# Performance work log

Hardware: AMD Instinct MI355X
Metric: run time of the kernel (lower is better)

## Reference

```python
import jax, jax.numpy as jnp
import numpy as np

N_HEAD = 12
N_EMBD = 768


def setup_inputs() -> dict:
    key = jax.random.key(0)
    k1, k2, k3, k4, k5 = jax.random.split(key, 5)
    B, T, C = 4, 2048, N_EMBD
    s = 0.02
    x = jax.random.normal(k1, (B, T, C), dtype=jnp.float32)
    w_attn = jax.random.normal(k2, (C, 3 * C), dtype=jnp.float32) * s
    b_attn = jnp.zeros((3 * C,), dtype=jnp.float32)
    w_proj = jax.random.normal(k3, (C, C), dtype=jnp.float32) * s
    b_proj = jnp.zeros((C,), dtype=jnp.float32)
    return {"x": x, "w_attn": w_attn, "b_attn": b_attn, "w_proj": w_proj, "b_proj": b_proj}


def reference(x, w_attn, b_attn, w_proj, b_proj):
    # dropout omitted (eval mode / dropout=0.0)
    B, T, C = x.shape
    H = N_HEAD
    D = C // H  # head dim
    qkv = x @ w_attn + b_attn                      # [B,T,3C]
    q, k, v = jnp.split(qkv, 3, axis=-1)
    q = q.reshape(B, T, H, D).transpose(0, 2, 1, 3)  # [B,H,T,D]
    k = k.reshape(B, T, H, D).transpose(0, 2, 1, 3)
    v = v.reshape(B, T, H, D).transpose(0, 2, 1, 3)
    att = jnp.einsum('bhqd,bhkd->bhqk', q, k) * (1.0 / np.sqrt(D))  # [B,H,T,T]
    causal = jnp.tril(jnp.ones((T, T), dtype=bool))
    att = jnp.where(causal[None, None], att, -jnp.inf)
    att = jax.nn.softmax(att, axis=-1)
    y = jnp.einsum('bhqk,bhkd->bhqd', att, v)      # [B,H,T,D]
    y = y.transpose(0, 2, 1, 3).reshape(B, T, C)
    return y @ w_proj + b_proj
```

## Files before the change

### kernel.cpp

```cpp
#include <hip/hip_runtime.h>
#include <stdint.h>

typedef unsigned short ushort_t;

#define T_SEQ 2048
#define BATCH 4
#define NHEAD 12
#define CEMB 768
#define HDIM 64
#define C3 2304

__device__ __forceinline__ ushort_t f2b_hw(float f) {
  union { __bf16 h; ushort_t u; } p;
  p.h = (__bf16)f;
  return p.u;
}
__device__ __forceinline__ uint32_t pkbf16(float lo, float hi) {
  union { __bf16 h[2]; uint32_t u; } p;
  p.h[0] = (__bf16)lo; p.h[1] = (__bf16)hi;
  return p.u;
}

typedef __attribute__((address_space(3))) unsigned int lds_u32_t;
typedef const __attribute__((address_space(1))) unsigned int glb_u32_t;
__device__ __forceinline__ void async_cp16(const void* g, void* l) {
  __builtin_amdgcn_global_load_lds((glb_u32_t*)g, (lds_u32_t*)l, 16, 0, 0);
}

__global__ __launch_bounds__(256) void prep_k(const float* __restrict__ x, ushort_t* __restrict__ xb,
                                              const float* __restrict__ wa, ushort_t* __restrict__ wT,
                                              const float* __restrict__ wp, ushort_t* __restrict__ wpT) {
  const int blk = blockIdx.x;
  const int tid = threadIdx.x;
  if (blk < 3072) {
    const int i = blk * 256 + tid;
    float4 a = ((const float4*)x)[2 * i];
    float4 b = ((const float4*)x)[2 * i + 1];
    uint4 v;
    v.x = pkbf16(a.x, a.y); v.y = pkbf16(a.z, a.w);
    v.z = pkbf16(b.x, b.y); v.w = pkbf16(b.z, b.w);
    ((uint4*)xb)[i] = v;
    return;
  }
  __shared__ ushort_t tile[32][33];
  const float* in; ushort_t* out; int R, C, bx, by;
  if (blk < 4800) {
    const int t = blk - 3072;
    in = wa; out = wT; R = CEMB; C = C3;
    bx = t % 72; by = t / 72;
  } else {
    const int t = blk - 4800;
    in = wp; out = wpT; R = CEMB; C = CEMB;
    bx = t % 24; by = t / 24;
  }
  const int tx = tid & 31, ty = tid >> 5;
  const int c0 = bx * 32, r0 = by * 32;
  for (int i = ty; i < 32; i += 8)
    tile[i][tx] = f2b_hw(in[(size_t)(r0 + i) * C + c0 + tx]);
  __syncthreads();
  for (int i = ty; i < 32; i += 8)
    out[(size_t)(c0 + i) * R + r0 + tx] = tile[tx][i];
}

typedef __bf16 bf16x8 __attribute__((ext_vector_type(8)));
typedef float f32x4 __attribute__((ext_vector_type(4)));

template <bool OUTF, int BM>
__global__ __launch_bounds__(256) void gemm_bt(const ushort_t* __restrict__ A,
                                               const ushort_t* __restrict__ Bt,
                                               const float* __restrict__ bias,
                                               void* __restrict__ Cv,
                                               int M, int N, int K) {
  constexpr int TM = BM / 32;
  __shared__ ushort_t As[BM * 32];
  __shared__ ushort_t Bs[128 * 32];
  const int tid = threadIdx.x;
  const int m0 = blockIdx.y * BM, n0 = blockIdx.x * 128;
  const int wid = tid >> 6, lane = tid & 63;
  const int quad = lane >> 4, l15 = lane & 15;
  const int wm = (wid >> 1) * (BM / 2), wn = (wid & 1) * 64;
  f32x4 acc[TM][4] = {};

  const int e0 = tid * 8;
  const int r0s = e0 >> 5, c0s = e0 & 31;
  const int e1 = e0 + 2048;
  const int r1s = e1 >> 5, c1s = e1 & 31;

  for (int k0 = 0; k0 < K; k0 += 32) {
    __syncthreads();
    async_cp16(&A[(size_t)(m0 + r0s) * K + k0 + c0s], &As[e0]);
    if constexpr (BM == 128)
      async_cp16(&A[(size_t)(m0 + r1s) * K + k0 + c1s], &As[e1]);
    async_cp16(&Bt[(size_t)(n0 + r0s) * K + k0 + c0s], &Bs[e0]);
    async_cp16(&Bt[(size_t)(n0 + r1s) * K + k0 + c1s], &Bs[e1]);
    __syncthreads();
    bf16x8 af[TM], bfr[4];
#pragma unroll
    for (int t = 0; t < TM; t++)
      af[t] = *(const bf16x8*)&As[(wm + t * 16 + l15) * 32 + quad * 8];
#pragma unroll
    for (int t = 0; t < 4; t++)
      bfr[t] = *(const bf16x8*)&Bs[(wn + t * 16 + l15) * 32 + quad * 8];
#pragma unroll
    for (int tm = 0; tm < TM; tm++)
#pragma unroll
      for (int tn = 0; tn < 4; tn++)
        acc[tm][tn] = __builtin_amdgcn_mfma_f32_16x16x32_bf16(af[tm], bfr[tn], acc[tm][tn], 0, 0, 0);
  }

#pragma unroll
  for (int tm = 0; tm < TM; tm++) {
    const int row = m0 + wm + tm * 16 + quad * 4;
#pragma unroll
    for (int tn = 0; tn < 4; tn++) {
      const int col = n0 + wn + tn * 16 + l15;
      const float bv = bias[col];
#pragma unroll
      for (int rr = 0; rr < 4; rr++) {
        if constexpr (OUTF)
          ((float*)Cv)[(size_t)(row + rr) * N + col] = acc[tm][tn][rr] + bv;
        else
          ((ushort_t*)Cv)[(size_t)(row + rr) * N + col] = f2b_hw(acc[tm][tn][rr] + bv);
      }
    }
  }
}

#define PSTR 72

__device__ __forceinline__ void commit_v(ushort_t* __restrict__ vt, int vd0, int vpair,
                                         uint4 pV0, uint4 pV1) {
  union { uint32_t u[4]; uint4 v; } a, c;
  a.v = pV0; c.v = pV1;
#pragma unroll
  for (int j = 0; j < 8; j++) {
    uint32_t pk = __builtin_amdgcn_perm(c.u[j >> 1], a.u[j >> 1],
                                        (j & 1) ? 0x07060302u : 0x05040100u);
    *(uint32_t*)&vt[(vd0 + j) * PSTR + 2 * vpair] = pk;
  }
}

__global__ __launch_bounds__(256) void attn_mfma_k(const ushort_t* __restrict__ qkv,
                                                   ushort_t* __restrict__ y) {
  __shared__ ushort_t Ksm[2][2][64 * 32];
  __shared__ ushort_t Vt[2][64 * PSTR];
  __shared__ ushort_t Plds[4][32 * PSTR];

  const int jj = blockIdx.x;
  const int h = blockIdx.y, b = blockIdx.z;
  const int tid = threadIdx.x;
  const int w = tid >> 6, lane = tid & 63;
  const int quad = lane >> 4, l15 = lane & 15;

  const int e0 = tid * 8;
  const int k_key = e0 >> 5, k_col = e0 & 31;
  const int vpair = tid & 31, vd0 = (tid >> 5) * 8;
  const ushort_t* kbase = qkv + ((size_t)(b * T_SEQ) + k_key) * C3 + CEMB + h * HDIM + k_col;
  const ushort_t* vbase = qkv + ((size_t)(b * T_SEQ) + 2 * vpair) * C3 + 2 * CEMB + h * HDIM + vd0;
  const size_t step = (size_t)64 * C3;

  int koff[4], voff[4], poffR[2], poffW[2];
#pragma unroll
  for (int m = 0; m < 4; m++) koff[m] = (m * 16 + l15) * 32 + quad * 8;
#pragma unroll
  for (int nd = 0; nd < 4; nd++) voff[nd] = (nd * 16 + l15) * PSTR + quad * 8;
#pragma unroll
  for (int n = 0; n < 2; n++) {
    poffR[n] = (n * 16 + l15) * PSTR + quad * 8;
    poffW[n] = (n * 16 + l15) * PSTR + quad * 4;
  }

  const float C2 = 0.18033688011112042f;

  for (int ph = 0; ph < 2; ++ph) {
    const int qt = ph ? (15 - jj) : jj;
    const int nkt = 2 * qt + 2;
    const int qw = qt * 128 + w * 32;

    bf16x8 qB[2][2];
#pragma unroll
    for (int n = 0; n < 2; n++)
#pragma unroll
      for (int kb = 0; kb < 2; kb++)
        qB[n][kb] = *(const bf16x8*)&qkv[((size_t)(b * T_SEQ + qw + n * 16 + l15)) * C3 +
                                         h * HDIM + kb * 32 + quad * 8];

    f32x4 o2[4][2] = {};
    float m_i[2] = {-3e38f, -3e38f}, l_i[2] = {0.f, 0.f};

    __syncthreads();

    const ushort_t* kp = kbase;
    const ushort_t* vp = vbase;
    uint4 pV0 = *(const uint4*)vp, pV1 = *(const uint4*)(vp + C3);
    async_cp16(kp, &Ksm[0][0][e0]);
    async_cp16(kp + 32, &Ksm[0][1][e0]);
    commit_v(Vt[0], vd0, vpair, pV0, pV1);
    vp += step;
    pV0 = *(const uint4*)vp; pV1 = *(const uint4*)(vp + C3);

    for (int kt = 0; kt < nkt; ++kt) {
      __syncthreads();
      if (kt + 1 < nkt) {
        const int nb = (kt + 1) & 1;
        kp += step;
        async_cp16(kp, &Ksm[nb][0][e0]);
        async_cp16(kp + 32, &Ksm[nb][1][e0]);
        commit_v(Vt[nb], vd0, vpair, pV0, pV1);
        if (kt + 2 < nkt) {
          vp += step;
          pV0 = *(const uint4*)vp; pV1 = *(const uint4*)(vp + C3);
        }
      }
      const int cb = kt & 1;

      if (kt * 64 <= qw + 31) {
        bf16x8 kA[4][2];
#pragma unroll
        for (int m = 0; m < 4; m++) {
          kA[m][0] = *(const bf16x8*)&Ksm[cb][0][koff[m]];
          kA[m][1] = *(const bf16x8*)&Ksm[cb][1][koff[m]];
        }
        f32x4 st[4][2] = {};
#pragma unroll
        for (int m = 0; m < 4; m++)
#pragma unroll
          for (int n = 0; n < 2; n++) {
            st[m][n] = __builtin_amdgcn_mfma_f32_16x16x32_bf16(kA[m][0], qB[n][0], st[m][n], 0, 0, 0);
            st[m][n] = __builtin_amdgcn_mfma_f32_16x16x32_bf16(kA[m][1], qB[n][1], st[m][n], 0, 0, 0);
          }

        if (kt * 64 + 63 > qw) {
#pragma unroll
          for (int m = 0; m < 4; m++)
#pragma unroll
            for (int r = 0; r < 4; r++) {
              const int keyg = kt * 64 + m * 16 + quad * 4 + r;
#pragma unroll
              for (int n = 0; n < 2; n++) {
                const int qg = qw + n * 16 + l15;
                if (keyg > qg) st[m][n][r] = -3e38f;
              }
            }
        }

        float al[2];
#pragma unroll
        for (int n = 0; n < 2; n++) {
          float mx = st[0][n][0];
#pragma unroll
          for (int m = 0; m < 4; m++)
#pragma unroll
            for (int r = 0; r < 4; r++) mx = fmaxf(mx, st[m][n][r]);
          mx = fmaxf(mx, __shfl_xor(mx, 16, 64));
          mx = fmaxf(mx, __shfl_xor(mx, 32, 64));
          const float mn = fmaxf(m_i[n], mx);
          al[n] = exp2f((m_i[n] - mn) * C2);
          m_i[n] = mn;
          const float mnc = mn * C2;
          float ls = 0.f;
#pragma unroll
          for (int m = 0; m < 4; m++)
#pragma unroll
            for (int r = 0; r < 4; r++) {
              float p = exp2f(fmaf(st[m][n][r], C2, -mnc));
              st[m][n][r] = p;
              ls += p;
            }
          ls += __shfl_xor(ls, 16, 64);
          ls += __shfl_xor(ls, 32, 64);
          l_i[n] = l_i[n] * al[n] + ls;
        }

#pragma unroll
        for (int n = 0; n < 2; n++) {
#pragma unroll
          for (int m = 0; m < 4; m++) {
            uint2 pk;
            pk.x = pkbf16(st[m][n][0], st[m][n][1]);
            pk.y = pkbf16(st[m][n][2], st[m][n][3]);
            *(uint2*)&Plds[w][poffW[n] + m * 16] = pk;
          }
#pragma unroll
          for (int nd = 0; nd < 4; nd++)
#pragma unroll
            for (int r = 0; r < 4; r++) o2[nd][n][r] *= al[n];
        }

        asm volatile("s_waitcnt lgkmcnt(0)" ::: "memory");

        bf16x8 ap[2][2], bv[4][2];
#pragma unroll
        for (int n = 0; n < 2; n++)
#pragma unroll
          for (int kb = 0; kb < 2; kb++)
            ap[n][kb] = *(const bf16x8*)&Plds[w][poffR[n] + kb * 32];
#pragma unroll
        for (int nd = 0; nd < 4; nd++)
#pragma unroll
          for (int kb = 0; kb < 2; kb++)
            bv[nd][kb] = *(const bf16x8*)&Vt[cb][voff[nd] + kb * 32];
#pragma unroll
        for (int nd = 0; nd < 4; nd++)
#pragma unroll
          for (int n = 0; n < 2; n++) {
            o2[nd][n] = __builtin_amdgcn_mfma_f32_16x16x32_bf16(bv[nd][0], ap[n][0], o2[nd][n], 0, 0, 0);
            o2[nd][n] = __builtin_amdgcn_mfma_f32_16x16x32_bf16(bv[nd][1], ap[n][1], o2[nd][n], 0, 0, 0);
          }
      }
    }

#pragma unroll
    for (int n = 0; n < 2; n++) {
      const float inv = 1.0f / l_i[n];
      const int qg = qw + n * 16 + l15;
      ushort_t* yp = y + ((size_t)(b * T_SEQ + qg)) * CEMB + h * HDIM + quad * 4;
#pragma unroll
      for (int nd = 0; nd < 4; nd++) {
        uint2 pk;
        pk.x = pkbf16(o2[nd][n][0] * inv, o2[nd][n][1] * inv);
        pk.y = pkbf16(o2[nd][n][2] * inv, o2[nd][n][3] * inv);
        *(uint2*)(yp + nd * 16) = pk;
      }
    }
  }
}

extern "C" void kernel_launch(void* const* d_in, const int* in_sizes, int n_in,
                              void* d_out, int out_size, void* d_ws, size_t ws_size,
                              hipStream_t stream) {
  const float* x      = (const float*)d_in[0];
  const float* w_attn = (const float*)d_in[1];
  const float* b_attn = (const float*)d_in[2];
  const float* w_proj = (const float*)d_in[3];
  const float* b_proj = (const float*)d_in[4];
  float* out = (float*)d_out;

  char* ws = (char*)d_ws;
  ushort_t* qkv = (ushort_t*)ws;
  ushort_t* y   = qkv + (size_t)8192 * 2304;
  ushort_t* xb  = y + (size_t)8192 * 768;
  ushort_t* wT  = xb + (size_t)8192 * 768;
  ushort_t* wpT = wT + (size_t)2304 * 768;

  prep_k<<<5376, 256, 0, stream>>>(x, xb, w_attn, wT, w_proj, wpT);

  gemm_bt<false, 128><<<dim3(C3 / 128, 8192 / 128), 256, 0, stream>>>(xb, wT, b_attn, qkv, 8192, C3, CEMB);

  attn_mfma_k<<<dim3(8, NHEAD, BATCH), 256, 0, stream>>>(qkv, y);

  gemm_bt<true, 64><<<dim3(CEMB / 128, 8192 / 64), 256, 0, stream>>>(y, wpT, b_proj, out, 8192, CEMB, CEMB);
}
```

Baseline: 256.9 us.

## Shrink attention query tile to 64 rows and double GEMM K-step to 64

The attention kernel now gives each block 64 query rows (16 per wave) instead of 128, and launches twice as many blocks (16x12x4). Causal pairing is preserved and the masking becomes a simple diagonal-tile check, which raises parallelism across the GPU. In exchange, each K/V tile loaded into LDS is reused by fewer queries. Separately, the GEMM now stages two 32-wide K slices per barrier pair, halving barrier count at the cost of doubled LDS usage.

```diff
diff --git a/kernel.cpp b/kernel.cpp
--- a/kernel.cpp
+++ b/kernel.cpp
@@ -72,8 +72,8 @@
                                                void* __restrict__ Cv,
                                                int M, int N, int K) {
   constexpr int TM = BM / 32;
-  __shared__ ushort_t As[BM * 32];
-  __shared__ ushort_t Bs[128 * 32];
+  __shared__ ushort_t As[2 * BM * 32];
+  __shared__ ushort_t Bs[2 * 128 * 32];
   const int tid = threadIdx.x;
   const int m0 = blockIdx.y * BM, n0 = blockIdx.x * 128;
   const int wid = tid >> 6, lane = tid & 63;
@@ -86,26 +86,36 @@
   const int e1 = e0 + 2048;
   const int r1s = e1 >> 5, c1s = e1 & 31;
 
-  for (int k0 = 0; k0 < K; k0 += 32) {
+  for (int k0 = 0; k0 < K; k0 += 64) {
     __syncthreads();
-    async_cp16(&A[(size_t)(m0 + r0s) * K + k0 + c0s], &As[e0]);
-    if constexpr (BM == 128)
-      async_cp16(&A[(size_t)(m0 + r1s) * K + k0 + c1s], &As[e1]);
-    async_cp16(&Bt[(size_t)(n0 + r0s) * K + k0 + c0s], &Bs[e0]);
-    async_cp16(&Bt[(size_t)(n0 + r1s) * K + k0 + c1s], &Bs[e1]);
+#pragma unroll
+    for (int p = 0; p < 2; p++) {
+      const int kc = k0 + p * 32;
+      async_cp16(&A[(size_t)(m0 + r0s) * K + kc + c0s], &As[p * BM * 32 + e0]);
+      if constexpr (BM == 128)
+        async_cp16(&A[(size_t)(m0 + r1s) * K + kc + c1s], &As[p * BM * 32 + e1]);
+      async_cp16(&Bt[(size_t)(n0 + r0s) * K + kc + c0s], &Bs[p * 128 * 32 + e0]);
+      async_cp16(&Bt[(size_t)(n0 + r1s) * K + kc + c1s], &Bs[p * 128 * 32 + e1]);
+    }
     __syncthreads();
-    bf16x8 af[TM], bfr[4];
+    bf16x8 af[TM][2], bfr[4][2];
 #pragma unroll
     for (int t = 0; t < TM; t++)
-      af[t] = *(const bf16x8*)&As[(wm + t * 16 + l15) * 32 + quad * 8];
+#pragma unroll
+      for (int p = 0; p < 2; p++)
+        af[t][p] = *(const bf16x8*)&As[p * BM * 32 + (wm + t * 16 + l15) * 32 + quad * 8];
 #pragma unroll
     for (int t = 0; t < 4; t++)
-      bfr[t] = *(const bf16x8*)&Bs[(wn + t * 16 + l15) * 32 + quad * 8];
-#pragma unroll
-    for (int tm = 0; tm < TM; tm++)
-#pragma unroll
-      for (int tn = 0; tn < 4; tn++)
-        acc[tm][tn] = __builtin_amdgcn_mfma_f32_16x16x32_bf16(af[tm], bfr[tn], acc[tm][tn], 0, 0, 0);
+#pragma unroll
+      for (int p = 0; p < 2; p++)
+        bfr[t][p] = *(const bf16x8*)&Bs[p * 128 * 32 + (wn + t * 16 + l15) * 32 + quad * 8];
+#pragma unroll
+    for (int p = 0; p < 2; p++)
+#pragma unroll
+      for (int tm = 0; tm < TM; tm++)
+#pragma unroll
+        for (int tn = 0; tn < 4; tn++)
+          acc[tm][tn] = __builtin_amdgcn_mfma_f32_16x16x32_bf16(af[tm][p], bfr[tn][p], acc[tm][tn], 0, 0, 0);
   }
 
 #pragma unroll
@@ -144,7 +154,7 @@
                                                    ushort_t* __restrict__ y) {
   __shared__ ushort_t Ksm[2][2][64 * 32];
   __shared__ ushort_t Vt[2][64 * PSTR];
-  __shared__ ushort_t Plds[4][32 * PSTR];
+  __shared__ ushort_t Plds[4][16 * PSTR];
 
   const int jj = blockIdx.x;
   const int h = blockIdx.y, b = blockIdx.z;
@@ -153,40 +163,35 @@
   const int quad = lane >> 4, l15 = lane & 15;
 
   const int e0 = tid * 8;
-  const int k_key = e0 >> 5, k_col = e0 & 31;
   const int vpair = tid & 31, vd0 = (tid >> 5) * 8;
-  const ushort_t* kbase = qkv + ((size_t)(b * T_SEQ) + k_key) * C3 + CEMB + h * HDIM + k_col;
+  const ushort_t* kbase = qkv + ((size_t)(b * T_SEQ) + (e0 >> 5)) * C3 + CEMB + h * HDIM + (e0 & 31);
   const ushort_t* vbase = qkv + ((size_t)(b * T_SEQ) + 2 * vpair) * C3 + 2 * CEMB + h * HDIM + vd0;
   const size_t step = (size_t)64 * C3;
 
-  int koff[4], voff[4], poffR[2], poffW[2];
+  int koff[4], voff[4];
 #pragma unroll
   for (int m = 0; m < 4; m++) koff[m] = (m * 16 + l15) * 32 + quad * 8;
 #pragma unroll
   for (int nd = 0; nd < 4; nd++) voff[nd] = (nd * 16 + l15) * PSTR + quad * 8;
-#pragma unroll
-  for (int n = 0; n < 2; n++) {
-    poffR[n] = (n * 16 + l15) * PSTR + quad * 8;
-    poffW[n] = (n * 16 + l15) * PSTR + quad * 4;
-  }
+  const int poffR = l15 * PSTR + quad * 8;
+  const int poffW = l15 * PSTR + quad * 4;
+  const int qloc = 16 * w + l15;
 
   const float C2 = 0.18033688011112042f;
 
   for (int ph = 0; ph < 2; ++ph) {
-    const int qt = ph ? (15 - jj) : jj;
-    const int nkt = 2 * qt + 2;
-    const int qw = qt * 128 + w * 32;
-
-    bf16x8 qB[2][2];
-#pragma unroll
-    for (int n = 0; n < 2; n++)
-#pragma unroll
-      for (int kb = 0; kb < 2; kb++)
-        qB[n][kb] = *(const bf16x8*)&qkv[((size_t)(b * T_SEQ + qw + n * 16 + l15)) * C3 +
-                                         h * HDIM + kb * 32 + quad * 8];
-
-    f32x4 o2[4][2] = {};
-    float m_i[2] = {-3e38f, -3e38f}, l_i[2] = {0.f, 0.f};
+    const int qt = ph ? (31 - jj) : jj;
+    const int nkt = qt + 1;
+    const int qw = qt * 64 + w * 16;
+
+    bf16x8 qB[2];
+#pragma unroll
+    for (int kb = 0; kb < 2; kb++)
+      qB[kb] = *(const bf16x8*)&qkv[((size_t)(b * T_SEQ + qw + l15)) * C3 +
+                                    h * HDIM + kb * 32 + quad * 8];
+
+    f32x4 o2[4] = {};
+    float m_i = -3e38f, l_i = 0.f;
 
     __syncthreads();
 
@@ -214,112 +219,90 @@
       }
       const int cb = kt & 1;
 
-      if (kt * 64 <= qw + 31) {
-        bf16x8 kA[4][2];
-#pragma unroll
-        for (int m = 0; m < 4; m++) {
-          kA[m][0] = *(const bf16x8*)&Ksm[cb][0][koff[m]];
-          kA[m][1] = *(const bf16x8*)&Ksm[cb][1][koff[m]];
+      bf16x8 kA[4][2];
+#pragma unroll
+      for (int m = 0; m < 4; m++) {
+        kA[m][0] = *(const bf16x8*)&Ksm[cb][0][koff[m]];
+        kA[m][1] = *(const bf16x8*)&Ksm[cb][1][koff[m]];
+      }
+      f32x4 st[4] = {};
+#pragma unroll
+      for (int m = 0; m < 4; m++) {
+        st[m] = __builtin_amdgcn_mfma_f32_16x16x32_bf16(kA[m][0], qB[0], st[m], 0, 0, 0);
+        st[m] = __builtin_amdgcn_mfma_f32_16x16x32_bf16(kA[m][1], qB[1], st[m], 0, 0, 0);
+      }
+
+      if (kt == qt) {
+#pragma unroll
+        for (int m = 0; m < 4; m++)
+#pragma unroll
+          for (int r = 0; r < 4; r++)
+            if (m * 16 + quad * 4 + r > qloc) st[m][r] = -3e38f;
+      }
+
+      float mx = st[0][0];
+#pragma unroll
+      for (int m = 0; m < 4; m++)
+#pragma unroll
+        for (int r = 0; r < 4; r++) mx = fmaxf(mx, st[m][r]);
+      mx = fmaxf(mx, __shfl_xor(mx, 16, 64));
+      mx = fmaxf(mx, __shfl_xor(mx, 32, 64));
+      const float mn = fmaxf(m_i, mx);
+      const float al = exp2f((m_i - mn) * C2);
+      m_i = mn;
+      const float mnc = mn * C2;
+      float ls = 0.f;
+#pragma unroll
+      for (int m = 0; m < 4; m++)
+#pragma unroll
+        for (int r = 0; r < 4; r++) {
+          float p = exp2f(fmaf(st[m][r], C2, -mnc));
+          st[m][r] = p;
+          ls += p;
         }
-        f32x4 st[4][2] = {};
-#pragma unroll
-        for (int m = 0; m < 4; m++)
-#pragma unroll
-          for (int n = 0; n < 2; n++) {
-            st[m][n] = __builtin_amdgcn_mfma_f32_16x16x32_bf16(kA[m][0], qB[n][0], st[m][n], 0, 0, 0);
-            st[m][n] = __builtin_amdgcn_mfma_f32_16x16x32_bf16(kA[m][1], qB[n][1], st[m][n], 0, 0, 0);
-          }
-
-        if (kt * 64 + 63 > qw) {
-#pragma unroll
-          for (int m = 0; m < 4; m++)
-#pragma unroll
-            for (int r = 0; r < 4; r++) {
-              const int keyg = kt * 64 + m * 16 + quad * 4 + r;
-#pragma unroll
-              for (int n = 0; n < 2; n++) {
-                const int qg = qw + n * 16 + l15;
-                if (keyg > qg) st[m][n][r] = -3e38f;
-              }
-            }
-        }
-
-        float al[2];
-#pragma unroll
-        for (int n = 0; n < 2; n++) {
-          float mx = st[0][n][0];
-#pragma unroll
-          for (int m = 0; m < 4; m++)
-#pragma unroll
-            for (int r = 0; r < 4; r++) mx = fmaxf(mx, st[m][n][r]);
-          mx = fmaxf(mx, __shfl_xor(mx, 16, 64));
-          mx = fmaxf(mx, __shfl_xor(mx, 32, 64));
-          const float mn = fmaxf(m_i[n], mx);
-          al[n] = exp2f((m_i[n] - mn) * C2);
-          m_i[n] = mn;
-          const float mnc = mn * C2;
-          float ls = 0.f;
-#pragma unroll
-          for (int m = 0; m < 4; m++)
-#pragma unroll
-            for (int r = 0; r < 4; r++) {
-              float p = exp2f(fmaf(st[m][n][r], C2, -mnc));
-              st[m][n][r] = p;
-              ls += p;
-            }
-          ls += __shfl_xor(ls, 16, 64);
-          ls += __shfl_xor(ls, 32, 64);
-          l_i[n] = l_i[n] * al[n] + ls;
-        }
-
-#pragma unroll
-        for (int n = 0; n < 2; n++) {
-#pragma unroll
-          for (int m = 0; m < 4; m++) {
-            uint2 pk;
-            pk.x = pkbf16(st[m][n][0], st[m][n][1]);
-            pk.y = pkbf16(st[m][n][2], st[m][n][3]);
-            *(uint2*)&Plds[w][poffW[n] + m * 16] = pk;
-          }
-#pragma unroll
-          for (int nd = 0; nd < 4; nd++)
-#pragma unroll
-            for (int r = 0; r < 4; r++) o2[nd][n][r] *= al[n];
-        }
-
-        asm volatile("s_waitcnt lgkmcnt(0)" ::: "memory");
-
-        bf16x8 ap[2][2], bv[4][2];
-#pragma unroll
-        for (int n = 0; n < 2; n++)
-#pragma unroll
-          for (int kb = 0; kb < 2; kb++)
-            ap[n][kb] = *(const bf16x8*)&Plds[w][poffR[n] + kb * 32];
-#pragma unroll
-        for (int nd = 0; nd < 4; nd++)
-#pragma unroll
-          for (int kb = 0; kb < 2; kb++)
-            bv[nd][kb] = *(const bf16x8*)&Vt[cb][voff[nd] + kb * 32];
-#pragma unroll
-        for (int nd = 0; nd < 4; nd++)
-#pragma unroll
-          for (int n = 0; n < 2; n++) {
-            o2[nd][n] = __builtin_amdgcn_mfma_f32_16x16x32_bf16(bv[nd][0], ap[n][0], o2[nd][n], 0, 0, 0);
-            o2[nd][n] = __builtin_amdgcn_mfma_f32_16x16x32_bf16(bv[nd][1], ap[n][1], o2[nd][n], 0, 0, 0);
-          }
+      ls += __shfl_xor(ls, 16, 64);
+      ls += __shfl_xor(ls, 32, 64);
+      l_i = l_i * al + ls;
+
+#pragma unroll
+      for (int m = 0; m < 4; m++) {
+        uint2 pk;
+        pk.x = pkbf16(st[m][0], st[m][1]);
+        pk.y = pkbf16(st[m][2], st[m][3]);
+        *(uint2*)&Plds[w][poffW + m * 16] = pk;
+      }
+#pragma unroll
+      for (int nd = 0; nd < 4; nd++)
+#pragma unroll
+        for (int r = 0; r < 4; r++) o2[nd][r] *= al;
+
+      asm volatile("s_waitcnt lgkmcnt(0)" ::: "memory");
+
+      bf16x8 ap[2], bv[4][2];
+#pragma unroll
+      for (int kb = 0; kb < 2; kb++)
+        ap[kb] = *(const bf16x8*)&Plds[w][poffR + kb * 32];
+#pragma unroll
+      for (int nd = 0; nd < 4; nd++)
+#pragma unroll
+        for (int kb = 0; kb < 2; kb++)
+          bv[nd][kb] = *(const bf16x8*)&Vt[cb][voff[nd] + kb * 32];
+#pragma unroll
+      for (int nd = 0; nd < 4; nd++) {
+        o2[nd] = __builtin_amdgcn_mfma_f32_16x16x32_bf16(bv[nd][0], ap[0], o2[nd], 0, 0, 0);
+        o2[nd] = __builtin_amdgcn_mfma_f32_16x16x32_bf16(bv[nd][1], ap[1], o2[nd], 0, 0, 0);
       }
     }
 
-#pragma unroll
-    for (int n = 0; n < 2; n++) {
-      const float inv = 1.0f / l_i[n];
-      const int qg = qw + n * 16 + l15;
+    {
+      const float inv = 1.0f / l_i;
+      const int qg = qw + l15;
       ushort_t* yp = y + ((size_t)(b * T_SEQ + qg)) * CEMB + h * HDIM + quad * 4;
 #pragma unroll
       for (int nd = 0; nd < 4; nd++) {
         uint2 pk;
-        pk.x = pkbf16(o2[nd][n][0] * inv, o2[nd][n][1] * inv);
-        pk.y = pkbf16(o2[nd][n][2] * inv, o2[nd][n][3] * inv);
+        pk.x = pkbf16(o2[nd][0] * inv, o2[nd][1] * inv);
+        pk.y = pkbf16(o2[nd][2] * inv, o2[nd][3] * inv);
         *(uint2*)(yp + nd * 16) = pk;
       }
     }
@@ -347,7 +330,7 @@
 
   gemm_bt<false, 128><<<dim3(C3 / 128, 8192 / 128), 256, 0, stream>>>(xb, wT, b_attn, qkv, 8192, C3, CEMB);
 
-  attn_mfma_k<<<dim3(8, NHEAD, BATCH), 256, 0, stream>>>(qkv, y);
+  attn_mfma_k<<<dim3(16, NHEAD, BATCH), 256, 0, stream>>>(qkv, y);
 
   gemm_bt<true, 64><<<dim3(CEMB / 128, 8192 / 64), 256, 0, stream>>>(y, wpT, b_proj, out, 8192, CEMB, CEMB);
 }
```

After: 231.9 us. 9.7% less time.
